# Kernel optimization log

Measured on AMD Instinct MI355X. Metric: run time of the kernel, lower is better.

The kernel has to match this reference:

```python
import jax, jax.numpy as jnp
import numpy as np

CAPACITY = 8_388_608  # 2**23, power of two -> leftmost_leaf == capacity
N_UPDATES = 1_048_576  # 2**20


def setup_inputs() -> dict:
    key = jax.random.key(0)
    k1, k2, k3 = jax.random.split(key, 3)
    # Existing tree buffer; values[1] is root, values[CAPACITY:2*CAPACITY] are leaves.
    tree_values = jax.random.uniform(k1, (2 * CAPACITY,), dtype=jnp.float32)
    # Distinct leaf indices in [0, CAPACITY): torch scatter-assign with duplicate
    # indices is nondeterministic, so the meaningful case is distinct indices.
    indices = jax.random.permutation(k2, CAPACITY)[:N_UPDATES].astype(jnp.int32)
    values = jax.random.uniform(k3, (N_UPDATES,), dtype=jnp.float32)
    return {"tree_values": tree_values, "indices": indices, "values": values}


def reference(tree_values, indices, values):
    """SegmentTree.__setitem__ with op=add: set leaves, propagate sums to root.

    Returns the updated (2*capacity,) tree buffer.
    """
    capacity = tree_values.shape[0] // 2  # static python int
    depth = int(capacity).bit_length() - 1  # log2(capacity) levels to the root
    # _index_to_leaf: with power-of-two capacity, leaf = idx + capacity (no wrap).
    leaf = indices.astype(jnp.int32) + capacity
    tree = tree_values.at[leaf].set(values)
    idx = leaf
    # Original does torch.unique(idx//2) per level purely as an optimization;
    # duplicate parents recompute the identical value, so plain scatter-set of
    # op(left_child, right_child) is the same math and jit-friendly.
    for _ in range(depth):
        idx = idx // 2
        parent = tree[2 * idx] + tree[2 * idx + 1]
        tree = tree.at[idx].set(parent)
    return tree
```

## Files before the change

kernel.cpp:

```cpp
#include <hip/hip_runtime.h>


typedef unsigned int uint;
typedef unsigned char uchar;
typedef unsigned long long ull;

#define NBINS 1024
#define BCAP  2048

__device__ __forceinline__ ull pc64(ull c) {
    ull x = (c | (c >> 1)) & 0x5555555555555555ull;
    x = (x | (x >> 1))  & 0x3333333333333333ull;
    x = (x | (x >> 2))  & 0x0F0F0F0F0F0F0F0Full;
    x = (x | (x >> 4))  & 0x00FF00FF00FF00FFull;
    x = (x | (x >> 8))  & 0x0000FFFF0000FFFFull;
    x = (x | (x >> 16)) & 0x00000000FFFFFFFFull;
    return x;
}

__global__ __launch_bounds__(1024)
void bin_kernel(const int* __restrict__ idx,
                const float* __restrict__ val,
                uint* __restrict__ cnt,
                uint2* __restrict__ bins) {
    __shared__ uint hist[NBINS];
    __shared__ uint rbase[NBINS];
    const int tid = threadIdx.x;
    hist[tid] = 0u;
    __syncthreads();

    const int g = blockIdx.x * 1024 + tid;
    int4   j4 = ((const int4*)idx)[g];
    float4 v4 = ((const float4*)val)[g];
    uint  j[4] = { (uint)j4.x, (uint)j4.y, (uint)j4.z, (uint)j4.w };
    float v[4] = { v4.x, v4.y, v4.z, v4.w };

    #pragma unroll
    for (int e = 0; e < 4; ++e) atomicAdd(&hist[j[e] >> 13], 1u);
    __syncthreads();

    uint h = hist[tid];
    rbase[tid] = h ? atomicAdd(&cnt[tid], h) : 0u;
    hist[tid] = 0u;
    __syncthreads();

    #pragma unroll
    for (int e = 0; e < 4; ++e) {
        uint bin = j[e] >> 13;
        uint r = rbase[bin] + atomicAdd(&hist[bin], 1u);
        if (r < BCAP)
            bins[((size_t)bin << 11) + r] =
                make_uint2(j[e] & 8191u, __float_as_uint(v[e]));
    }
}

__global__ __launch_bounds__(1024)
void merge_kernel(const float* __restrict__ tree,
                  const uint* __restrict__ cnt,
                  const uint2* __restrict__ bins,
                  uint* __restrict__ l13v,
                  uint* __restrict__ l13f,
                  uint* __restrict__ done,
                  float* __restrict__ out, int C) {
    __shared__ float slv[8192];
    __shared__ uchar sfl[8192];
    __shared__ float s9v[16];
    __shared__ uint  s9d[16];
    __shared__ uint  sticket;
    __shared__ float s16v[16];
    __shared__ uint  s16d[16];

    const int b    = blockIdx.x;
    const int tid  = threadIdx.x;
    const int wv   = tid >> 6;
    const int lane = tid & 63;

    ((uint2*)sfl)[tid] = make_uint2(0u, 0u);
    __syncthreads();
    uint c = cnt[b];
    if (c > BCAP) c = BCAP;
    const uint2* mybin = bins + ((size_t)b << 11);
    for (uint k = tid; k < c; k += 1024u) {
        uint2 e = mybin[k];
        slv[e.x] = __uint_as_float(e.y);
        sfl[e.x] = 1;
    }
    __syncthreads();

    const int leaf0  = tid * 8;
    const int gleaf0 = b * 8192 + leaf0;

    uint2 fw = *(const uint2*)&sfl[leaf0];
    float4 la = *(const float4*)&slv[leaf0];
    float4 lb = *(const float4*)&slv[leaf0 + 4];
    float4 ta = *(const float4*)(tree + C + gleaf0);
    float4 tb = *(const float4*)(tree + C + gleaf0 + 4);

    float l0 = (fw.x & 0x000000FFu) ? la.x : ta.x;
    float l1 = (fw.x & 0x0000FF00u) ? la.y : ta.y;
    float l2 = (fw.x & 0x00FF0000u) ? la.z : ta.z;
    float l3 = (fw.x & 0xFF000000u) ? la.w : ta.w;
    float l4 = (fw.y & 0x000000FFu) ? lb.x : tb.x;
    float l5 = (fw.y & 0x0000FF00u) ? lb.y : tb.y;
    float l6 = (fw.y & 0x00FF0000u) ? lb.z : tb.z;
    float l7 = (fw.y & 0xFF000000u) ? lb.w : tb.w;

    *(float4*)(out + C + gleaf0)     = make_float4(l0, l1, l2, l3);
    *(float4*)(out + C + gleaf0 + 4) = make_float4(l4, l5, l6, l7);

    uint d10 = (fw.x & 0x0000FFFFu) != 0u;
    uint d11 = (fw.x & 0xFFFF0000u) != 0u;
    uint d12 = (fw.y & 0x0000FFFFu) != 0u;
    uint d13 = (fw.y & 0xFFFF0000u) != 0u;
    float4 t1 = *(const float4*)(tree + (C >> 1) + (gleaf0 >> 1));
    float4 v1;
    v1.x = d10 ? l0 + l1 : t1.x;
    v1.y = d11 ? l2 + l3 : t1.y;
    v1.z = d12 ? l4 + l5 : t1.z;
    v1.w = d13 ? l6 + l7 : t1.w;
    *(float4*)(out + (C >> 1) + (gleaf0 >> 1)) = v1;

    float2 t2 = *(const float2*)(tree + (C >> 2) + (gleaf0 >> 2));
    uint d20 = d10 | d11, d21 = d12 | d13;
    float2 v2;
    v2.x = d20 ? v1.x + v1.y : t2.x;
    v2.y = d21 ? v1.z + v1.w : t2.y;
    *(float2*)(out + (C >> 2) + (gleaf0 >> 2)) = v2;

    float t3v = tree[(C >> 3) + (gleaf0 >> 3)];
    uint d3 = d20 | d21;
    float v = d3 ? v2.x + v2.y : t3v;
    out[(C >> 3) + (gleaf0 >> 3)] = v;

    const int r = b * 16 + wv;
    ull m = __ballot(d3 != 0u);
    #pragma unroll
    for (int lvl = 4; lvl <= 9; ++lvl) {
        float a  = __shfl(v, 2 * lane, 64);
        float bb = __shfl(v, 2 * lane + 1, 64);
        m = pc64(m);
        int n = 64 >> (lvl - 3);
        if (lane < n) {
            int node = (C >> lvl) + (r << (9 - lvl)) + lane;
            uint dd = (uint)(m >> lane) & 1u;
            v = dd ? a + bb : tree[node];
            out[node] = v;
        }
    }
    if (lane == 0) { s9v[wv] = v; s9d[wv] = (uint)(m & 1ull); }
    __syncthreads();

    if (wv == 0) {
        float vv = lane < 16 ? s9v[lane] : 0.f;
        uint dd  = lane < 16 ? s9d[lane] : 0u;
        ull mm = __ballot(dd != 0u);
        #pragma unroll
        for (int lvl = 10; lvl <= 13; ++lvl) {
            float a  = __shfl(vv, 2 * lane, 64);
            float bb = __shfl(vv, 2 * lane + 1, 64);
            mm = pc64(mm);
            int n = 1 << (13 - lvl);
            if (lane < n) {
                int node = (C >> lvl) + (b << (13 - lvl)) + lane;
                uint d2 = (uint)(mm >> lane) & 1u;
                vv = d2 ? a + bb : tree[node];
                out[node] = vv;
            }
        }
        if (lane == 0) {
            uint o1 = atomicExch(&l13v[b], __float_as_uint(vv));
            uint o2 = atomicExch(&l13f[b], (uint)(mm & 1ull));
            asm volatile("" : : "v"(o1), "v"(o2));
            sticket = atomicAdd(done, 1u);
        }
    }
    __syncthreads();
    if (sticket != (uint)gridDim.x - 1u) return;

    {
        const int w2 = tid >> 6;
        float tv = __uint_as_float(atomicOr(&l13v[tid], 0u));
        uint  td = atomicOr(&l13f[tid], 0u);

        ull m2 = __ballot(td != 0u);
        #pragma unroll
        for (int M = 512; M >= 16; M >>= 1) {
            float a  = __shfl(tv, 2 * lane, 64);
            float bb = __shfl(tv, 2 * lane + 1, 64);
            m2 = pc64(m2);
            int nw = M >> 4;
            if (lane < nw) {
                int node = M + nw * w2 + lane;
                uint dd = (uint)(m2 >> lane) & 1u;
                tv = dd ? a + bb : tree[node];
                out[node] = tv;
            }
        }
        if (lane == 0) { s16v[w2] = tv; s16d[w2] = (uint)(m2 & 1ull); }
        __syncthreads();

        if (w2 == 0) {
            float vv2 = lane < 16 ? s16v[lane] : 0.f;
            uint dd2  = lane < 16 ? s16d[lane] : 0u;
            ull mm2 = __ballot(dd2 != 0u);
            #pragma unroll
            for (int M = 8; M >= 1; M >>= 1) {
                float a  = __shfl(vv2, 2 * lane, 64);
                float bb = __shfl(vv2, 2 * lane + 1, 64);
                mm2 = pc64(mm2);
                if (lane < M) {
                    uint d2 = (uint)(mm2 >> lane) & 1u;
                    vv2 = d2 ? a + bb : tree[M + lane];
                    out[M + lane] = vv2;
                }
            }
            if (lane == 0) out[0] = tree[0];
        }
    }
}

extern "C" void kernel_launch(void* const* d_in, const int* in_sizes, int n_in,
                              void* d_out, int out_size, void* d_ws, size_t ws_size,
                              hipStream_t stream) {
    const float* tree    = (const float*)d_in[0];
    const int*   indices = (const int*)d_in[1];
    const float* values  = (const float*)d_in[2];
    float* out = (float*)d_out;

    const int two_cap = in_sizes[0];
    const int C       = two_cap >> 1;
    const int nupd    = in_sizes[1];

    uchar* ws = (uchar*)d_ws;
    uint*  cnt  = (uint*)ws;
    uint*  done = (uint*)(ws + 4096);
    uint*  l13v = (uint*)(ws + 8192);
    uint*  l13f = (uint*)(ws + 12288);
    uint2* bins = (uint2*)(ws + 32768);

    hipMemsetAsync(ws, 0, 4160, stream);
    bin_kernel<<<nupd / 4096, 1024, 0, stream>>>(indices, values, cnt, bins);
    merge_kernel<<<C / 8192, 1024, 0, stream>>>(tree, cnt, bins, l13v, l13f,
                                                done, out, C);
}
```

Measured before the change: 145.8 us.

## Shrink merge blocks to 256 threads with four leaf chunks per thread

The merge kernel now launches 256-thread blocks. Each thread processes four 8-leaf chunks, and the per-level shuffle reductions interleave four independent wave reductions. Bin entries are read two at a time as uint4. The final root-reduction block is reshaped to fit 256 threads by folding the first two levels in registers. This trades thread-level parallelism for more per-thread ILP and fewer barriers per thread. The large shared arrays may now limit how many blocks fit on each CU.

```diff
diff --git a/kernel.cpp b/kernel.cpp
--- a/kernel.cpp
+++ b/kernel.cpp
@@ -54,7 +54,7 @@
     }
 }
 
-__global__ __launch_bounds__(1024)
+__global__ __launch_bounds__(256)
 void merge_kernel(const float* __restrict__ tree,
                   const uint* __restrict__ cnt,
                   const uint2* __restrict__ bins,
@@ -63,7 +63,7 @@
                   uint* __restrict__ done,
                   float* __restrict__ out, int C) {
     __shared__ float slv[8192];
-    __shared__ uchar sfl[8192];
+    __shared__ uint  sflw[2048];
     __shared__ float s9v[16];
     __shared__ uint  s9d[16];
     __shared__ uint  sticket;
@@ -74,80 +74,107 @@
     const int tid  = threadIdx.x;
     const int wv   = tid >> 6;
     const int lane = tid & 63;
-
-    ((uint2*)sfl)[tid] = make_uint2(0u, 0u);
-    __syncthreads();
+    uchar* sfl = (uchar*)sflw;
+
+    #pragma unroll
+    for (int i = 0; i < 8; ++i) sflw[i * 256 + tid] = 0u;
+    __syncthreads();
+
     uint c = cnt[b];
     if (c > BCAP) c = BCAP;
-    const uint2* mybin = bins + ((size_t)b << 11);
-    for (uint k = tid; k < c; k += 1024u) {
-        uint2 e = mybin[k];
+    const uint2* mybin  = bins + ((size_t)b << 11);
+    const uint4* mybin4 = (const uint4*)mybin;
+    for (uint k = tid; k < (c >> 1); k += 256u) {
+        uint4 e2 = mybin4[k];
+        slv[e2.x] = __uint_as_float(e2.y);
+        sfl[e2.x] = 1;
+        slv[e2.z] = __uint_as_float(e2.w);
+        sfl[e2.z] = 1;
+    }
+    if ((c & 1u) && tid == 0) {
+        uint2 e = mybin[c - 1];
         slv[e.x] = __uint_as_float(e.y);
         sfl[e.x] = 1;
     }
     __syncthreads();
 
-    const int leaf0  = tid * 8;
-    const int gleaf0 = b * 8192 + leaf0;
-
-    uint2 fw = *(const uint2*)&sfl[leaf0];
-    float4 la = *(const float4*)&slv[leaf0];
-    float4 lb = *(const float4*)&slv[leaf0 + 4];
-    float4 ta = *(const float4*)(tree + C + gleaf0);
-    float4 tb = *(const float4*)(tree + C + gleaf0 + 4);
-
-    float l0 = (fw.x & 0x000000FFu) ? la.x : ta.x;
-    float l1 = (fw.x & 0x0000FF00u) ? la.y : ta.y;
-    float l2 = (fw.x & 0x00FF0000u) ? la.z : ta.z;
-    float l3 = (fw.x & 0xFF000000u) ? la.w : ta.w;
-    float l4 = (fw.y & 0x000000FFu) ? lb.x : tb.x;
-    float l5 = (fw.y & 0x0000FF00u) ? lb.y : tb.y;
-    float l6 = (fw.y & 0x00FF0000u) ? lb.z : tb.z;
-    float l7 = (fw.y & 0xFF000000u) ? lb.w : tb.w;
-
-    *(float4*)(out + C + gleaf0)     = make_float4(l0, l1, l2, l3);
-    *(float4*)(out + C + gleaf0 + 4) = make_float4(l4, l5, l6, l7);
-
-    uint d10 = (fw.x & 0x0000FFFFu) != 0u;
-    uint d11 = (fw.x & 0xFFFF0000u) != 0u;
-    uint d12 = (fw.y & 0x0000FFFFu) != 0u;
-    uint d13 = (fw.y & 0xFFFF0000u) != 0u;
-    float4 t1 = *(const float4*)(tree + (C >> 1) + (gleaf0 >> 1));
-    float4 v1;
-    v1.x = d10 ? l0 + l1 : t1.x;
-    v1.y = d11 ? l2 + l3 : t1.y;
-    v1.z = d12 ? l4 + l5 : t1.z;
-    v1.w = d13 ? l6 + l7 : t1.w;
-    *(float4*)(out + (C >> 1) + (gleaf0 >> 1)) = v1;
-
-    float2 t2 = *(const float2*)(tree + (C >> 2) + (gleaf0 >> 2));
-    uint d20 = d10 | d11, d21 = d12 | d13;
-    float2 v2;
-    v2.x = d20 ? v1.x + v1.y : t2.x;
-    v2.y = d21 ? v1.z + v1.w : t2.y;
-    *(float2*)(out + (C >> 2) + (gleaf0 >> 2)) = v2;
-
-    float t3v = tree[(C >> 3) + (gleaf0 >> 3)];
-    uint d3 = d20 | d21;
-    float v = d3 ? v2.x + v2.y : t3v;
-    out[(C >> 3) + (gleaf0 >> 3)] = v;
-
-    const int r = b * 16 + wv;
-    ull m = __ballot(d3 != 0u);
+    float vL[4];
+    ull   mk[4];
+    #pragma unroll
+    for (int it = 0; it < 4; ++it) {
+        const int leaf0  = it * 2048 + tid * 8;
+        const int gleaf0 = b * 8192 + leaf0;
+
+        uint2 fw = *(const uint2*)&sfl[leaf0];
+        float4 la = *(const float4*)&slv[leaf0];
+        float4 lb = *(const float4*)&slv[leaf0 + 4];
+        float4 ta = *(const float4*)(tree + C + gleaf0);
+        float4 tb = *(const float4*)(tree + C + gleaf0 + 4);
+
+        float l0 = (fw.x & 0x000000FFu) ? la.x : ta.x;
+        float l1 = (fw.x & 0x0000FF00u) ? la.y : ta.y;
+        float l2 = (fw.x & 0x00FF0000u) ? la.z : ta.z;
+        float l3 = (fw.x & 0xFF000000u) ? la.w : ta.w;
+        float l4 = (fw.y & 0x000000FFu) ? lb.x : tb.x;
+        float l5 = (fw.y & 0x0000FF00u) ? lb.y : tb.y;
+        float l6 = (fw.y & 0x00FF0000u) ? lb.z : tb.z;
+        float l7 = (fw.y & 0xFF000000u) ? lb.w : tb.w;
+
+        *(float4*)(out + C + gleaf0)     = make_float4(l0, l1, l2, l3);
+        *(float4*)(out + C + gleaf0 + 4) = make_float4(l4, l5, l6, l7);
+
+        uint d10 = (fw.x & 0x0000FFFFu) != 0u;
+        uint d11 = (fw.x & 0xFFFF0000u) != 0u;
+        uint d12 = (fw.y & 0x0000FFFFu) != 0u;
+        uint d13 = (fw.y & 0xFFFF0000u) != 0u;
+        float4 t1 = *(const float4*)(tree + (C >> 1) + (gleaf0 >> 1));
+        float4 v1;
+        v1.x = d10 ? l0 + l1 : t1.x;
+        v1.y = d11 ? l2 + l3 : t1.y;
+        v1.z = d12 ? l4 + l5 : t1.z;
+        v1.w = d13 ? l6 + l7 : t1.w;
+        *(float4*)(out + (C >> 1) + (gleaf0 >> 1)) = v1;
+
+        float2 t2 = *(const float2*)(tree + (C >> 2) + (gleaf0 >> 2));
+        uint d20 = d10 | d11, d21 = d12 | d13;
+        float2 v2;
+        v2.x = d20 ? v1.x + v1.y : t2.x;
+        v2.y = d21 ? v1.z + v1.w : t2.y;
+        *(float2*)(out + (C >> 2) + (gleaf0 >> 2)) = v2;
+
+        float t3v = tree[(C >> 3) + (gleaf0 >> 3)];
+        uint d3 = d20 | d21;
+        float v = d3 ? v2.x + v2.y : t3v;
+        out[(C >> 3) + (gleaf0 >> 3)] = v;
+
+        vL[it] = v;
+        mk[it] = __ballot(d3 != 0u);
+    }
+
     #pragma unroll
     for (int lvl = 4; lvl <= 9; ++lvl) {
-        float a  = __shfl(v, 2 * lane, 64);
-        float bb = __shfl(v, 2 * lane + 1, 64);
-        m = pc64(m);
         int n = 64 >> (lvl - 3);
-        if (lane < n) {
-            int node = (C >> lvl) + (r << (9 - lvl)) + lane;
-            uint dd = (uint)(m >> lane) & 1u;
-            v = dd ? a + bb : tree[node];
-            out[node] = v;
-        }
-    }
-    if (lane == 0) { s9v[wv] = v; s9d[wv] = (uint)(m & 1ull); }
+        #pragma unroll
+        for (int it = 0; it < 4; ++it) {
+            float a  = __shfl(vL[it], 2 * lane, 64);
+            float bb = __shfl(vL[it], 2 * lane + 1, 64);
+            mk[it] = pc64(mk[it]);
+            if (lane < n) {
+                int r = b * 16 + it * 4 + wv;
+                int node = (C >> lvl) + (r << (9 - lvl)) + lane;
+                uint dd = (uint)(mk[it] >> lane) & 1u;
+                vL[it] = dd ? a + bb : tree[node];
+                out[node] = vL[it];
+            }
+        }
+    }
+    if (lane == 0) {
+        #pragma unroll
+        for (int it = 0; it < 4; ++it) {
+            s9v[it * 4 + wv] = vL[it];
+            s9d[it * 4 + wv] = (uint)(mk[it] & 1ull);
+        }
+    }
     __syncthreads();
 
     if (wv == 0) {
@@ -179,16 +206,30 @@
 
     {
         const int w2 = tid >> 6;
-        float tv = __uint_as_float(atomicOr(&l13v[tid], 0u));
-        uint  td = atomicOr(&l13f[tid], 0u);
-
-        ull m2 = __ballot(td != 0u);
-        #pragma unroll
-        for (int M = 512; M >= 16; M >>= 1) {
+        float s13[4]; uint f13[4];
+        #pragma unroll
+        for (int k = 0; k < 4; ++k) {
+            s13[k] = __uint_as_float(atomicOr(&l13v[4 * tid + k], 0u));
+            f13[k] = atomicOr(&l13f[4 * tid + k], 0u);
+        }
+
+        float2 t14 = *(const float2*)(tree + 512 + 2 * tid);
+        uint dA = f13[0] | f13[1], dB = f13[2] | f13[3];
+        float vA = dA ? s13[0] + s13[1] : t14.x;
+        float vB = dB ? s13[2] + s13[3] : t14.y;
+        *(float2*)(out + 512 + 2 * tid) = make_float2(vA, vB);
+
+        uint d = dA | dB;
+        float tv = d ? vA + vB : tree[256 + tid];
+        out[256 + tid] = tv;
+
+        ull m2 = __ballot(d != 0u);
+        #pragma unroll
+        for (int M = 128; M >= 16; M >>= 1) {
             float a  = __shfl(tv, 2 * lane, 64);
             float bb = __shfl(tv, 2 * lane + 1, 64);
             m2 = pc64(m2);
-            int nw = M >> 4;
+            int nw = M >> 2;
             if (lane < nw) {
                 int node = M + nw * w2 + lane;
                 uint dd = (uint)(m2 >> lane) & 1u;
@@ -196,22 +237,23 @@
                 out[node] = tv;
             }
         }
-        if (lane == 0) { s16v[w2] = tv; s16d[w2] = (uint)(m2 & 1ull); }
+        if (lane < 4) { s16v[4 * w2 + lane] = tv;
+                        s16d[4 * w2 + lane] = (uint)(m2 >> lane) & 1u; }
         __syncthreads();
 
         if (w2 == 0) {
-            float vv2 = lane < 16 ? s16v[lane] : 0.f;
-            uint dd2  = lane < 16 ? s16d[lane] : 0u;
-            ull mm2 = __ballot(dd2 != 0u);
+            float vv = lane < 16 ? s16v[lane] : 0.f;
+            uint dd  = lane < 16 ? s16d[lane] : 0u;
+            ull mm = __ballot(dd != 0u);
             #pragma unroll
             for (int M = 8; M >= 1; M >>= 1) {
-                float a  = __shfl(vv2, 2 * lane, 64);
-                float bb = __shfl(vv2, 2 * lane + 1, 64);
-                mm2 = pc64(mm2);
+                float a  = __shfl(vv, 2 * lane, 64);
+                float bb = __shfl(vv, 2 * lane + 1, 64);
+                mm = pc64(mm);
                 if (lane < M) {
-                    uint d2 = (uint)(mm2 >> lane) & 1u;
-                    vv2 = d2 ? a + bb : tree[M + lane];
-                    out[M + lane] = vv2;
+                    uint d2 = (uint)(mm >> lane) & 1u;
+                    vv = d2 ? a + bb : tree[M + lane];
+                    out[M + lane] = vv;
                 }
             }
             if (lane == 0) out[0] = tree[0];
@@ -240,6 +282,6 @@
 
     hipMemsetAsync(ws, 0, 4160, stream);
     bin_kernel<<<nupd / 4096, 1024, 0, stream>>>(indices, values, cnt, bins);
-    merge_kernel<<<C / 8192, 1024, 0, stream>>>(tree, cnt, bins, l13v, l13f,
-                                                done, out, C);
-}
+    merge_kernel<<<NBINS, 256, 0, stream>>>(tree, cnt, bins, l13v, l13f,
+                                            done, out, C);
+}
```

New measurement: 154.7 us. +6.1%, slower.
